# Optimization experiments

Hardware: AMD Instinct MI355X
Metric: run time of the kernel (lower is better)

The kernel has to match this reference:

```python
import jax, jax.numpy as jnp
import numpy as np

COS_MARGIN = 0.35
ARC_MARGIN = 0.5
SCALE = 30.0
EPS = 1e-12

B, V = 2048, 32000


def setup_inputs() -> dict:
    key = jax.random.key(0)
    k1, k2 = jax.random.split(key)
    # logits are cosine similarities in [-1, 1]
    preds = jax.random.uniform(k1, (B, V), dtype=jnp.float32) * 2.0 - 1.0
    labels = jax.random.randint(k2, (B,), 0, V, dtype=jnp.int64)
    return {"preds": preds, "labels": labels}


def reference(preds, labels):
    # target cosine: preds[i, labels[i]]  (torch.diagonal(preds.T[labels]))
    target = jnp.take_along_axis(preds, labels[:, None], axis=1)[:, 0]
    theta = jnp.arccos(jnp.clip(target, -1.0 + EPS, 1.0 - EPS))
    theta = jnp.clip(theta, EPS, jnp.pi - EPS)  # 4*arctan(1) == pi
    numerator = SCALE * (jnp.cos(theta + ARC_MARGIN) - COS_MARGIN)  # [B]
    # sum of exp(scale * preds) over all classes except the target class
    cols = jnp.arange(preds.shape[1])  # [V]
    exp_all = jnp.exp(SCALE * preds)  # [B, V]
    sum_others = jnp.sum(jnp.where(cols[None, :] == labels[:, None], 0.0, exp_all), axis=1)
    denominator = jnp.exp(numerator) + sum_others
    return -jnp.mean(numerator - jnp.log(denominator))
```

## Files before the change

kernel.cpp:

```cpp
#include <hip/hip_runtime.h>
#include <math.h>

#define B_ROWS 2048
#define V_COLS 32000
#define SCALE_D 30.0
#define COS_MARGIN_D 0.35
#define ARC_MARGIN_D 0.5
#define EPS_D 1e-12
#define PI_D 3.14159265358979323846

#define LOG2E_X30 43.2808512266689022212f

typedef float f32x4 __attribute__((ext_vector_type(4)));

#define TPB 1024

__global__ __launch_bounds__(TPB) void cosarc_row_kernel(
    const float* __restrict__ preds,
    const int*   __restrict__ labels,
    float*       __restrict__ row_terms)
{
    const int row = blockIdx.x;
    const int tid = threadIdx.x;
    const float* rowp = preds + (size_t)row * V_COLS;
    const f32x4* rowp4 = (const f32x4*)rowp;
    const int NV4 = V_COLS / 4;

    float s0 = 0.f, s1 = 0.f, s2 = 0.f, s3 = 0.f;
    float s4 = 0.f, s5 = 0.f, s6 = 0.f, s7 = 0.f;

    int i = tid;
    for (; i + TPB < NV4; i += 2 * TPB) {
        f32x4 a = __builtin_nontemporal_load(&rowp4[i]);
        f32x4 b = __builtin_nontemporal_load(&rowp4[i + TPB]);
        s0 += __builtin_amdgcn_exp2f(a.x * LOG2E_X30);
        s1 += __builtin_amdgcn_exp2f(a.y * LOG2E_X30);
        s2 += __builtin_amdgcn_exp2f(a.z * LOG2E_X30);
        s3 += __builtin_amdgcn_exp2f(a.w * LOG2E_X30);
        s4 += __builtin_amdgcn_exp2f(b.x * LOG2E_X30);
        s5 += __builtin_amdgcn_exp2f(b.y * LOG2E_X30);
        s6 += __builtin_amdgcn_exp2f(b.z * LOG2E_X30);
        s7 += __builtin_amdgcn_exp2f(b.w * LOG2E_X30);
    }
    for (; i < NV4; i += TPB) {
        f32x4 a = __builtin_nontemporal_load(&rowp4[i]);
        s0 += __builtin_amdgcn_exp2f(a.x * LOG2E_X30);
        s1 += __builtin_amdgcn_exp2f(a.y * LOG2E_X30);
        s2 += __builtin_amdgcn_exp2f(a.z * LOG2E_X30);
        s3 += __builtin_amdgcn_exp2f(a.w * LOG2E_X30);
    }
    double sum = (double)(((s0 + s1) + (s2 + s3)) + ((s4 + s5) + (s6 + s7)));

    #pragma unroll
    for (int off = 32; off > 0; off >>= 1)
        sum += __shfl_down(sum, off, 64);

    __shared__ double wave_sums[TPB / 64];
    const int wave = tid >> 6;
    const int lane = tid & 63;
    if (lane == 0) wave_sums[wave] = sum;
    __syncthreads();

    if (tid == 0) {
        double total = 0.0;
        #pragma unroll
        for (int w = 0; w < TPB / 64; ++w) total += wave_sums[w];

        const float tgt_f = rowp[labels[row]];
        const double sum_others =
            total - (double)__builtin_amdgcn_exp2f(tgt_f * LOG2E_X30);

        double t = (double)tgt_f;
        t = fmin(fmax(t, -1.0 + EPS_D), 1.0 - EPS_D);
        double theta = acos(t);
        theta = fmin(fmax(theta, EPS_D), PI_D - EPS_D);
        const double numerator = SCALE_D * (cos(theta + ARC_MARGIN_D) - COS_MARGIN_D);
        const double denominator = exp(numerator) + sum_others;
        row_terms[row] = (float)(numerator - log(denominator));
    }
}

__global__ __launch_bounds__(256) void cosarc_reduce_kernel(
    const float* __restrict__ row_terms,
    float*       __restrict__ out)
{
    const int tid = threadIdx.x;
    double s = 0.0;
    for (int i = tid; i < B_ROWS; i += 256)
        s += (double)row_terms[i];

    #pragma unroll
    for (int off = 32; off > 0; off >>= 1)
        s += __shfl_down(s, off, 64);

    __shared__ double wave_sums[4];
    if ((tid & 63) == 0) wave_sums[tid >> 6] = s;
    __syncthreads();

    if (tid == 0) {
        double total = wave_sums[0] + wave_sums[1] + wave_sums[2] + wave_sums[3];
        out[0] = (float)(-(total / (double)B_ROWS));
    }
}

extern "C" void kernel_launch(void* const* d_in, const int* in_sizes, int n_in,
                              void* d_out, int out_size, void* d_ws, size_t ws_size,
                              hipStream_t stream)
{
    const float* preds  = (const float*)d_in[0];
    const int*   labels = (const int*)d_in[1];
    float*       out    = (float*)d_out;
    float*       ws     = (float*)d_ws;

    cosarc_row_kernel<<<B_ROWS, TPB, 0, stream>>>(preds, labels, ws);
    cosarc_reduce_kernel<<<1, 256, 0, stream>>>(ws, out);
}
```

Before: 326.9 us.

## Split each row across four blocks with fully unrolled preloaded loads

Each row is now split into four chunks handled by 256-thread blocks (8192 blocks total). Each thread issues all of its 7-8 vector loads up front before doing the exp work, instead of looping. Per-chunk partial sums and the target value go to workspace, and the per-row arcface math moves into the final single-block kernel. This aims to raise memory-level parallelism and occupancy on the bandwidth-bound 262MB read. It also drops the nontemporal load hint and adds a serial per-row transcendental cost in the final kernel.

```diff
diff --git a/kernel.cpp b/kernel.cpp
--- a/kernel.cpp
+++ b/kernel.cpp
@@ -13,49 +13,64 @@
 
 typedef float f32x4 __attribute__((ext_vector_type(4)));
 
-#define TPB 1024
 
-__global__ __launch_bounds__(TPB) void cosarc_row_kernel(
+#define TPB_A 256
+#define CHUNKS 4
+#define V4_CHUNK (V_COLS / 4 / CHUNKS)
+#define TAIL_T (V4_CHUNK - 7 * TPB_A)
+
+#define EXP30(x) __builtin_amdgcn_exp2f((x) * LOG2E_X30)
+
+__global__ __launch_bounds__(TPB_A, 8) void cosarc_partial_kernel(
     const float* __restrict__ preds,
     const int*   __restrict__ labels,
-    float*       __restrict__ row_terms)
+    double*      __restrict__ partials,
+    float*       __restrict__ tgts)
 {
-    const int row = blockIdx.x;
-    const int tid = threadIdx.x;
+    const int bid   = blockIdx.x;
+    const int row   = bid >> 2;
+    const int chunk = bid & 3;
+    const int tid   = threadIdx.x;
+
     const float* rowp = preds + (size_t)row * V_COLS;
-    const f32x4* rowp4 = (const f32x4*)rowp;
-    const int NV4 = V_COLS / 4;
+    const f32x4* p4   = (const f32x4*)rowp + chunk * V4_CHUNK;
 
-    float s0 = 0.f, s1 = 0.f, s2 = 0.f, s3 = 0.f;
-    float s4 = 0.f, s5 = 0.f, s6 = 0.f, s7 = 0.f;
+    f32x4 v0 = p4[tid];
+    f32x4 v1 = p4[tid + 1 * TPB_A];
+    f32x4 v2 = p4[tid + 2 * TPB_A];
+    f32x4 v3 = p4[tid + 3 * TPB_A];
+    f32x4 v4 = p4[tid + 4 * TPB_A];
+    f32x4 v5 = p4[tid + 5 * TPB_A];
+    f32x4 v6 = p4[tid + 6 * TPB_A];
+    const bool has8 = (tid < TAIL_T);
+    f32x4 v7 = {0.f, 0.f, 0.f, 0.f};
+    if (has8) v7 = p4[tid + 7 * TPB_A];
 
-    int i = tid;
-    for (; i + TPB < NV4; i += 2 * TPB) {
-        f32x4 a = __builtin_nontemporal_load(&rowp4[i]);
-        f32x4 b = __builtin_nontemporal_load(&rowp4[i + TPB]);
-        s0 += __builtin_amdgcn_exp2f(a.x * LOG2E_X30);
-        s1 += __builtin_amdgcn_exp2f(a.y * LOG2E_X30);
-        s2 += __builtin_amdgcn_exp2f(a.z * LOG2E_X30);
-        s3 += __builtin_amdgcn_exp2f(a.w * LOG2E_X30);
-        s4 += __builtin_amdgcn_exp2f(b.x * LOG2E_X30);
-        s5 += __builtin_amdgcn_exp2f(b.y * LOG2E_X30);
-        s6 += __builtin_amdgcn_exp2f(b.z * LOG2E_X30);
-        s7 += __builtin_amdgcn_exp2f(b.w * LOG2E_X30);
+    if (tid == 0) {
+        const int l  = labels[row];
+        const int c0 = chunk * (V_COLS / CHUNKS);
+        if (l >= c0 && l < c0 + (V_COLS / CHUNKS)) tgts[row] = rowp[l];
     }
-    for (; i < NV4; i += TPB) {
-        f32x4 a = __builtin_nontemporal_load(&rowp4[i]);
-        s0 += __builtin_amdgcn_exp2f(a.x * LOG2E_X30);
-        s1 += __builtin_amdgcn_exp2f(a.y * LOG2E_X30);
-        s2 += __builtin_amdgcn_exp2f(a.z * LOG2E_X30);
-        s3 += __builtin_amdgcn_exp2f(a.w * LOG2E_X30);
+
+    float sx, sy, sz, sw;
+    sx  = EXP30(v0.x); sy  = EXP30(v0.y); sz  = EXP30(v0.z); sw  = EXP30(v0.w);
+    sx += EXP30(v1.x); sy += EXP30(v1.y); sz += EXP30(v1.z); sw += EXP30(v1.w);
+    sx += EXP30(v2.x); sy += EXP30(v2.y); sz += EXP30(v2.z); sw += EXP30(v2.w);
+    sx += EXP30(v3.x); sy += EXP30(v3.y); sz += EXP30(v3.z); sw += EXP30(v3.w);
+    sx += EXP30(v4.x); sy += EXP30(v4.y); sz += EXP30(v4.z); sw += EXP30(v4.w);
+    sx += EXP30(v5.x); sy += EXP30(v5.y); sz += EXP30(v5.z); sw += EXP30(v5.w);
+    sx += EXP30(v6.x); sy += EXP30(v6.y); sz += EXP30(v6.z); sw += EXP30(v6.w);
+    if (has8) {
+        sx += EXP30(v7.x); sy += EXP30(v7.y); sz += EXP30(v7.z); sw += EXP30(v7.w);
     }
-    double sum = (double)(((s0 + s1) + (s2 + s3)) + ((s4 + s5) + (s6 + s7)));
+
+    double sum = (double)((sx + sy) + (sz + sw));
 
     #pragma unroll
     for (int off = 32; off > 0; off >>= 1)
         sum += __shfl_down(sum, off, 64);
 
-    __shared__ double wave_sums[TPB / 64];
+    __shared__ double wave_sums[TPB_A / 64];
     const int wave = tid >> 6;
     const int lane = tid & 63;
     if (lane == 0) wave_sums[wave] = sum;
@@ -64,11 +79,24 @@
     if (tid == 0) {
         double total = 0.0;
         #pragma unroll
-        for (int w = 0; w < TPB / 64; ++w) total += wave_sums[w];
+        for (int w = 0; w < TPB_A / 64; ++w) total += wave_sums[w];
+        partials[bid] = total;
+    }
+}
 
-        const float tgt_f = rowp[labels[row]];
-        const double sum_others =
-            total - (double)__builtin_amdgcn_exp2f(tgt_f * LOG2E_X30);
+__global__ __launch_bounds__(1024) void cosarc_final_kernel(
+    const double* __restrict__ partials,
+    const float*  __restrict__ tgts,
+    float*        __restrict__ out)
+{
+    const int tid = threadIdx.x;
+    double acc = 0.0;
+
+    for (int r = tid; r < B_ROWS; r += 1024) {
+        const double total = (partials[4 * r] + partials[4 * r + 1]) +
+                             (partials[4 * r + 2] + partials[4 * r + 3]);
+        const float tgt_f = tgts[r];
+        const double sum_others = total - (double)EXP30(tgt_f);
 
         double t = (double)tgt_f;
         t = fmin(fmax(t, -1.0 + EPS_D), 1.0 - EPS_D);
@@ -76,29 +104,21 @@
         theta = fmin(fmax(theta, EPS_D), PI_D - EPS_D);
         const double numerator = SCALE_D * (cos(theta + ARC_MARGIN_D) - COS_MARGIN_D);
         const double denominator = exp(numerator) + sum_others;
-        row_terms[row] = (float)(numerator - log(denominator));
+        acc += numerator - log(denominator);
     }
-}
-
-__global__ __launch_bounds__(256) void cosarc_reduce_kernel(
-    const float* __restrict__ row_terms,
-    float*       __restrict__ out)
-{
-    const int tid = threadIdx.x;
-    double s = 0.0;
-    for (int i = tid; i < B_ROWS; i += 256)
-        s += (double)row_terms[i];
 
     #pragma unroll
     for (int off = 32; off > 0; off >>= 1)
-        s += __shfl_down(s, off, 64);
+        acc += __shfl_down(acc, off, 64);
 
-    __shared__ double wave_sums[4];
-    if ((tid & 63) == 0) wave_sums[tid >> 6] = s;
+    __shared__ double wave_sums[16];
+    if ((tid & 63) == 0) wave_sums[tid >> 6] = acc;
     __syncthreads();
 
     if (tid == 0) {
-        double total = wave_sums[0] + wave_sums[1] + wave_sums[2] + wave_sums[3];
+        double total = 0.0;
+        #pragma unroll
+        for (int w = 0; w < 16; ++w) total += wave_sums[w];
         out[0] = (float)(-(total / (double)B_ROWS));
     }
 }
@@ -110,8 +130,10 @@
     const float* preds  = (const float*)d_in[0];
     const int*   labels = (const int*)d_in[1];
     float*       out    = (float*)d_out;
-    float*       ws     = (float*)d_ws;
 
-    cosarc_row_kernel<<<B_ROWS, TPB, 0, stream>>>(preds, labels, ws);
-    cosarc_reduce_kernel<<<1, 256, 0, stream>>>(ws, out);
+    double* partials = (double*)d_ws;
+    float*  tgts     = (float*)((char*)d_ws + B_ROWS * CHUNKS * sizeof(double));
+
+    cosarc_partial_kernel<<<B_ROWS * CHUNKS, TPB_A, 0, stream>>>(preds, labels, partials, tgts);
+    cosarc_final_kernel<<<1, 1024, 0, stream>>>(partials, tgts, out);
 }
```

After: 352.0 us. 7.7% more time.
